# Performance work log

Hardware: AMD Instinct MI355X
Metric: run time of the kernel (lower is better)

The kernel has to match this reference:

```python
import jax, jax.numpy as jnp
import numpy as np

N_F, N_C = 100000, 25000          # fine / coarse node counts
C_IN, C_OUT = 128, 128
E_POOL, E = 200000, 400000        # pooling edges, coarse point-point edges


def setup_inputs() -> dict:
    key = jax.random.key(0)
    ks = jax.random.split(key, 12)
    x = jax.random.normal(ks[0], (N_F, C_IN), jnp.float32)
    # pooling edges: src in fine graph, dst in coarse graph
    pool_src = jax.random.randint(ks[1], (E_POOL,), 0, N_F, dtype=jnp.int64)
    pool_dst = jax.random.randint(ks[2], (E_POOL,), 0, N_C, dtype=jnp.int64)
    pool_edge_index = jnp.stack([pool_src, pool_dst])
    pool_edge_attr = jax.random.uniform(ks[3], (E_POOL,), jnp.float32)
    # coarse point-point edges
    src = jax.random.randint(ks[4], (E,), 0, N_C, dtype=jnp.int64)
    dst = jax.random.randint(ks[5], (E,), 0, N_C, dtype=jnp.int64)
    edge_index = jnp.stack([src, dst])
    edge_attr = jax.random.uniform(ks[6], (E,), jnp.float32)
    s_in = 1.0 / np.sqrt(C_IN).astype(np.float32)
    s_out = 1.0 / np.sqrt(C_OUT).astype(np.float32)
    W1_root = jax.random.normal(ks[7], (C_IN, C_OUT), jnp.float32) * s_in
    W1_nb = jax.random.normal(ks[8], (C_IN, C_OUT), jnp.float32) * s_in
    b1 = jnp.zeros((C_OUT,), jnp.float32)
    W2_root = jax.random.normal(ks[9], (C_OUT, C_OUT), jnp.float32) * s_out
    W2_nb = jax.random.normal(ks[10], (C_OUT, C_OUT), jnp.float32) * s_out
    b2 = jnp.zeros((C_OUT,), jnp.float32)
    return {
        "x": x,
        "pool_edge_index": pool_edge_index,
        "pool_edge_attr": pool_edge_attr,
        "edge_index": edge_index,
        "edge_attr": edge_attr,
        "W1_root": W1_root, "W1_nb": W1_nb, "b1": b1,
        "W2_root": W2_root, "W2_nb": W2_nb, "b2": b2,
        "n_coarse": N_C,
    }


def _graph_conv(h, edge_index, edge_attr, W_root, W_nb, b, n_nodes):
    # GraphConv with edge weights: out = h @ W_root + scatter_add(w_e * (h[src] @ W_nb), dst) + b
    msg = edge_attr[:, None] * (h[edge_index[0]] @ W_nb)          # [E, C_out]
    agg = jax.ops.segment_sum(msg, edge_index[1], num_segments=n_nodes)
    return h @ W_root + agg + b


def reference(x, pool_edge_index, pool_edge_attr, edge_index, edge_attr,
              W1_root, W1_nb, b1, W2_root, W2_nb, b2, n_coarse):
    # CustomPoolingAdd: weighted scatter-add fine -> coarse
    pooled = jax.ops.segment_sum(pool_edge_attr[:, None] * x[pool_edge_index[0]],
                                 pool_edge_index[1], num_segments=n_coarse)  # [N_c, C_in]
    h = _graph_conv(pooled, edge_index, edge_attr, W1_root, W1_nb, b1, n_coarse)
    h = _graph_conv(h, edge_index, edge_attr, W2_root, W2_nb, b2, n_coarse)
    return h
```

## Files before the change

### kernel.cpp

```cpp
#include <hip/hip_runtime.h>

typedef __attribute__((ext_vector_type(8))) short   short8;
typedef __attribute__((ext_vector_type(8))) __bf16  bf16x8;
typedef __attribute__((ext_vector_type(4))) float   f32x4;

__device__ __forceinline__ float bf2f(unsigned short u) {
    union { unsigned int i; float f; } v; v.i = ((unsigned int)u) << 16; return v.f;
}
__device__ __forceinline__ unsigned short f2bf(float f) {
    union { float f; unsigned int i; } v; v.f = f;
    unsigned int r = v.i + 0x7fffu + ((v.i >> 16) & 1u);
    return (unsigned short)(r >> 16);
}

__device__ __forceinline__ int load_idx(const void* p, int is64, long long i) {
    return is64 ? (int)((const long long*)p)[i] : ((const int*)p)[i];
}
__device__ __forceinline__ float load_f(const void* p, int isbf, long long i) {
    return isbf ? bf2f(((const unsigned short*)p)[i]) : ((const float*)p)[i];
}

__device__ __forceinline__ int self_is64(const int* p) {
    int lane = threadIdx.x & 63;
    unsigned long long b = __ballot(p[2 * lane + 1] != 0);
    return b == 0ull;
}
__device__ __forceinline__ int self_isbf(const unsigned int* p) {
    int lane = threadIdx.x & 63;
    unsigned int lo = p[lane] & 0xFFFFu;
    int e = (int)((lo >> 7) & 0xFF);
    int ok = (lo == 0u) || (e >= 88 && e <= 141);
    return (__ballot(!ok) == 0ull) ? 1 : 0;
}

__global__ void detect_kernel(const int* __restrict__ pei, const int* __restrict__ ei,
                              const unsigned int* f0, const unsigned int* f1,
                              const unsigned int* f2, const unsigned int* f3,
                              const unsigned int* f4, const unsigned int* f5,
                              const unsigned int* f6, const unsigned int* f7,
                              const unsigned int* f8,
                              int* __restrict__ flags) {
    int lane = threadIdx.x & 63;
    unsigned long long ba = __ballot(pei[2 * lane + 1] != 0);
    unsigned long long bb = __ballot(ei[2 * lane + 1] != 0);
    const unsigned int* fa[9] = {f0, f1, f2, f3, f4, f5, f6, f7, f8};
    int bf[9];
    #pragma unroll
    for (int t = 0; t < 9; t++) {
        unsigned int lo = fa[t][lane] & 0xFFFFu;
        int e = (int)((lo >> 7) & 0xFF);
        int ok = (lo == 0u) || (e >= 88 && e <= 141);
        bf[t] = (__ballot(!ok) == 0ull) ? 1 : 0;
    }
    if (lane == 0) {
        flags[0] = (ba == 0ull);
        flags[1] = (bb == 0ull);
        #pragma unroll
        for (int t = 0; t < 9; t++) flags[2 + t] = bf[t];
    }
}

#define BKT_CAP 64
#define OVF_CAP 4096

__global__ void fillb_kernel(const void* __restrict__ pei, const void* __restrict__ pattr,
                             const void* __restrict__ ei, const void* __restrict__ eattr,
                             int* __restrict__ pcnt, int2* __restrict__ pbkt,
                             int* __restrict__ povfc, int4* __restrict__ povf,
                             int* __restrict__ ccnt, int2* __restrict__ cbkt,
                             int* __restrict__ covfc, int4* __restrict__ covf,
                             int Ep, int Ec) {
    long long g = (long long)blockIdx.x * 256 + threadIdx.x;
    if (g < Ep) {
        int is64 = self_is64((const int*)pei);
        int abf = self_isbf((const unsigned int*)pattr);
        int s = load_idx(pei, is64, g);
        int d = load_idx(pei, is64, (long long)Ep + g);
        float w = load_f(pattr, abf, g);
        int pos = atomicAdd(&pcnt[d], 1);
        if (pos < BKT_CAP) {
            pbkt[(long long)d * BKT_CAP + pos] = make_int2(s, __float_as_int(w));
        } else {
            int oi = atomicAdd(povfc, 1);
            if (oi < OVF_CAP) povf[oi] = make_int4(s, __float_as_int(w), d, 0);
        }
    } else if (g - Ep < Ec) {
        long long e = g - Ep;
        int is64 = self_is64((const int*)ei);
        int abf = self_isbf((const unsigned int*)eattr);
        int s = load_idx(ei, is64, e);
        int d = load_idx(ei, is64, (long long)Ec + e);
        float w = load_f(eattr, abf, e);
        int pos = atomicAdd(&ccnt[d], 1);
        if (pos < BKT_CAP) {
            cbkt[(long long)d * BKT_CAP + pos] = make_int2(s, __float_as_int(w));
        } else {
            int oi = atomicAdd(covfc, 1);
            if (oi < OVF_CAP) covf[oi] = make_int4(s, __float_as_int(w), d, 0);
        }
    }
}

__global__ void gatherb_kernel(const void* __restrict__ in,
                               const int* __restrict__ cnt,
                               const int2* __restrict__ bkt,
                               const int* __restrict__ ovfc,
                               const int4* __restrict__ ovf,
                               unsigned short* __restrict__ out, int NC,
                               int detectIn) {
    int d = blockIdx.x * 4 + (threadIdx.x >> 6);
    if (d >= NC) return;
    int lane = threadIdx.x & 63;
    int j1 = cnt[d]; if (j1 > BKT_CAP) j1 = BKT_CAP;
    const int2* row = bkt + (long long)d * BKT_CAP;
    float ax = 0.f, ay = 0.f;
    int bf = detectIn ? self_isbf((const unsigned int*)in) : 1;
    if (!bf) {
        const float* fin = (const float*)in;
        int c0 = lane * 2;
        int j = 0;
        for (; j + 4 <= j1; j += 4) {
            int2 e0 = row[j], e1 = row[j + 1], e2 = row[j + 2], e3 = row[j + 3];
            float w0 = __int_as_float(e0.y), w1 = __int_as_float(e1.y);
            float w2 = __int_as_float(e2.y), w3 = __int_as_float(e3.y);
            float2 v0 = *(const float2*)(fin + (long long)e0.x * 128 + c0);
            float2 v1 = *(const float2*)(fin + (long long)e1.x * 128 + c0);
            float2 v2 = *(const float2*)(fin + (long long)e2.x * 128 + c0);
            float2 v3 = *(const float2*)(fin + (long long)e3.x * 128 + c0);
            ax += w0 * v0.x + w1 * v1.x + w2 * v2.x + w3 * v3.x;
            ay += w0 * v0.y + w1 * v1.y + w2 * v2.y + w3 * v3.y;
        }
        for (; j < j1; j++) {
            int2 e = row[j];
            float w = __int_as_float(e.y);
            float2 v = *(const float2*)(fin + (long long)e.x * 128 + c0);
            ax += w * v.x; ay += w * v.y;
        }
        int novf = *ovfc;
        if (novf > 0) {
            if (novf > OVF_CAP) novf = OVF_CAP;
            for (int k = 0; k < novf; k++) {
                int4 e = ovf[k];
                if (e.z == d) {
                    float w = __int_as_float(e.y);
                    float2 v = *(const float2*)(fin + (long long)e.x * 128 + c0);
                    ax += w * v.x; ay += w * v.y;
                }
            }
        }
    } else {
        const unsigned int* uin = (const unsigned int*)in;
        int j = 0;
        for (; j + 4 <= j1; j += 4) {
            int2 e0 = row[j], e1 = row[j + 1], e2 = row[j + 2], e3 = row[j + 3];
            float w0 = __int_as_float(e0.y), w1 = __int_as_float(e1.y);
            float w2 = __int_as_float(e2.y), w3 = __int_as_float(e3.y);
            unsigned int v0 = uin[(long long)e0.x * 64 + lane];
            unsigned int v1 = uin[(long long)e1.x * 64 + lane];
            unsigned int v2 = uin[(long long)e2.x * 64 + lane];
            unsigned int v3 = uin[(long long)e3.x * 64 + lane];
            ax += w0 * bf2f((unsigned short)v0) + w1 * bf2f((unsigned short)v1)
                + w2 * bf2f((unsigned short)v2) + w3 * bf2f((unsigned short)v3);
            ay += w0 * bf2f((unsigned short)(v0 >> 16)) + w1 * bf2f((unsigned short)(v1 >> 16))
                + w2 * bf2f((unsigned short)(v2 >> 16)) + w3 * bf2f((unsigned short)(v3 >> 16));
        }
        for (; j < j1; j++) {
            int2 e = row[j];
            float w = __int_as_float(e.y);
            unsigned int v = uin[(long long)e.x * 64 + lane];
            ax += w * bf2f((unsigned short)v);
            ay += w * bf2f((unsigned short)(v >> 16));
        }
        int novf = *ovfc;
        if (novf > 0) {
            if (novf > OVF_CAP) novf = OVF_CAP;
            for (int k = 0; k < novf; k++) {
                int4 e = ovf[k];
                if (e.z == d) {
                    float w = __int_as_float(e.y);
                    unsigned int v = uin[(long long)e.x * 64 + lane];
                    ax += w * bf2f((unsigned short)v);
                    ay += w * bf2f((unsigned short)(v >> 16));
                }
            }
        }
    }
    unsigned int o = (unsigned int)f2bf(ax) | ((unsigned int)f2bf(ay) << 16);
    ((unsigned int*)out)[(long long)d * 64 + lane] = o;
}

__global__ void packw_kernel(const void* __restrict__ w1r, const void* __restrict__ w1n,
                             const void* __restrict__ w2r, const void* __restrict__ w2n,
                             unsigned short* __restrict__ wpack) {
    int gid = blockIdx.x * 256 + threadIdx.x;
    int layer = gid >> 15;
    int r = gid & 32767;
    int j = r & 7, lane = (r >> 3) & 63, ch = (r >> 9) & 7, ct = (r >> 12) & 7;
    int n = ct * 16 + (lane & 15);
    int k = ch * 32 + (lane >> 4) * 8 + j;
    const void* w;
    if (layer == 0) w = (k < 128) ? w1r : w1n;
    else            w = (k < 128) ? w2r : w2n;
    int fs = self_isbf((const unsigned int*)w);
    float v = load_f(w, fs, (long long)(k & 127) * 128 + n);
    wpack[gid] = f2bf(v);
}

__global__ __launch_bounds__(256, 4)
void gemm_mfma_kernel(const unsigned short* __restrict__ H,
                      const unsigned short* __restrict__ G,
                      const unsigned short* __restrict__ wpack,
                      const void* __restrict__ bias,
                      float* __restrict__ outF, unsigned short* __restrict__ outB,
                      int NC) {
    __shared__ unsigned short ldsA[64 * 264];
    int tid = threadIdx.x;
    long long r0 = (long long)blockIdx.x * 64;
    for (int i = tid; i < 4096; i += 256) {
        int mat = i >> 11;
        int flat = i & 2047;
        int row = flat >> 5;
        int c4 = flat & 31;
        long long r = r0 + row;
        const unsigned short* srcp = mat ? G : H;
        uint2 v = make_uint2(0u, 0u);
        if (r < NC) v = *(const uint2*)(srcp + r * 128 + c4 * 4);
        *(uint2*)&ldsA[row * 264 + mat * 128 + c4 * 4] = v;
    }
    __syncthreads();

    int wave = tid >> 6, lane = tid & 63;
    int m = lane & 15, quad = lane >> 4;
    int arow = wave * 16 + m;

    bf16x8 a[8];
    #pragma unroll
    for (int ch = 0; ch < 8; ch++) {
        short8 av = *(const short8*)&ldsA[arow * 264 + ch * 32 + quad * 8];
        a[ch] = __builtin_bit_cast(bf16x8, av);
    }

    f32x4 acc[8];
    #pragma unroll
    for (int ct = 0; ct < 8; ct++) acc[ct] = (f32x4){0.f, 0.f, 0.f, 0.f};

    #pragma unroll
    for (int ct = 0; ct < 8; ct++) {
        #pragma unroll
        for (int ch = 0; ch < 8; ch++) {
            short8 bv = *(const short8*)(wpack + ((ct * 8 + ch) * 64 + lane) * 8);
            acc[ct] = __builtin_amdgcn_mfma_f32_16x16x32_bf16(
                a[ch], __builtin_bit_cast(bf16x8, bv), acc[ct], 0, 0, 0);
        }
    }

    int bbf = self_isbf((const unsigned int*)bias);
    #pragma unroll
    for (int ct = 0; ct < 8; ct++) {
        int n = ct * 16 + m;
        float bv = load_f(bias, bbf, n);
        #pragma unroll
        for (int r = 0; r < 4; r++) {
            long long rr = r0 + wave * 16 + quad * 4 + r;
            if (rr < NC) {
                float val = acc[ct][r] + bv;
                if (outF) outF[rr * 128 + n] = val;
                else      outB[rr * 128 + n] = f2bf(val);
            }
        }
    }
}

__global__ void pool_scatter_kernel(const void* __restrict__ x, const void* __restrict__ pei,
                                    const void* __restrict__ pattr, const int* __restrict__ flags,
                                    float* __restrict__ pooled, int Ep, int CI) {
    int c = blockIdx.y * blockDim.x + threadIdx.x;
    if (c >= CI) return;
    int e = blockIdx.x;
    int is64 = flags[0], xbf = flags[2], abf = flags[3];
    int s = load_idx(pei, is64, e);
    int d = load_idx(pei, is64, (long long)Ep + e);
    float w = load_f(pattr, abf, e);
    float v = load_f(x, xbf, (long long)s * CI + c);
    atomicAdd(&pooled[(long long)d * CI + c], w * v);
}

__global__ void conv_scatter_kernel(const float* __restrict__ t, const void* __restrict__ ei,
                                    const void* __restrict__ attr, const int* __restrict__ flags,
                                    float* __restrict__ outacc, int Ec, int CO) {
    int c = blockIdx.y * blockDim.x + threadIdx.x;
    if (c >= CO) return;
    int e = blockIdx.x;
    int is64 = flags[1], abf = flags[4];
    int s = load_idx(ei, is64, e);
    int d = load_idx(ei, is64, (long long)Ec + e);
    float w = load_f(attr, abf, e);
    atomicAdd(&outacc[(long long)d * CO + c], w * t[(long long)s * CO + c]);
}

__global__ void gemm_kernel(const float* H, const void* __restrict__ Wr,
                            const void* __restrict__ Wn, const void* __restrict__ bias,
                            const int* __restrict__ flags, int fWr, int fWn, int fB,
                            float* out_root, float* out_t, int NC, int CI, int CO) {
    __shared__ float lds[4][1024];
    int wave = threadIdx.x >> 6;
    int lane = threadIdx.x & 63;
    int r = blockIdx.x * 4 + wave;
    if (r < NC) {
        const float* hrow = H + (long long)r * CI;
        for (int k = lane; k < CI; k += 64) lds[wave][k] = hrow[k];
    }
    __syncthreads();
    if (r >= NC) return;
    int wrbf = flags[fWr], wnbf = flags[fWn], bbf = flags[fB];
    for (int c0 = lane * 2; c0 < CO; c0 += 128) {
        int two = (c0 + 1 < CO);
        float ar0 = 0.f, ar1 = 0.f, an0 = 0.f, an1 = 0.f;
        for (int k = 0; k < CI; k++) {
            float h = lds[wave][k];
            ar0 += h * load_f(Wr, wrbf, (long long)k * CO + c0);
            an0 += h * load_f(Wn, wnbf, (long long)k * CO + c0);
            if (two) {
                ar1 += h * load_f(Wr, wrbf, (long long)k * CO + c0 + 1);
                an1 += h * load_f(Wn, wnbf, (long long)k * CO + c0 + 1);
            }
        }
        long long o = (long long)r * CO + c0;
        out_root[o] = ar0 + load_f(bias, bbf, c0);
        out_t[o] = an0;
        if (two) {
            out_root[o + 1] = ar1 + load_f(bias, bbf, c0 + 1);
            out_t[o + 1] = an1;
        }
    }
}

__global__ void to_out_kernel(const float* __restrict__ in, float* __restrict__ out, long long n) {
    long long stride = (long long)gridDim.x * blockDim.x;
    for (long long i = (long long)blockIdx.x * blockDim.x + threadIdx.x; i < n; i += stride)
        out[i] = in[i];
}

extern "C" void kernel_launch(void* const* d_in, const int* in_sizes, int n_in,
                              void* d_out, int out_size, void* d_ws, size_t ws_size,
                              hipStream_t stream) {
    const void* x = d_in[0]; const void* pei = d_in[1]; const void* pattr = d_in[2];
    const void* ei = d_in[3]; const void* eattr = d_in[4];
    const void* w1r = d_in[5]; const void* w1n = d_in[6]; const void* b1 = d_in[7];
    const void* w2r = d_in[8]; const void* w2n = d_in[9]; const void* b2 = d_in[10];

    long long CO = in_sizes[7];
    long long CI = CO > 0 ? in_sizes[5] / CO : 0;
    long long Ep = in_sizes[2];
    long long Ec = in_sizes[4];
    long long NC = CO > 0 ? (long long)out_size / CO : 0;
    int sane = (CO > 0 && CI > 0 && CI <= 1024 && CO <= 1024 &&
                CI * CO == in_sizes[5] && NC * CO == out_size &&
                Ep > 0 && Ec > 0 && in_sizes[0] % CI == 0);
    if (!sane) { CO = 128; CI = 128; Ep = 200000; Ec = 400000; NC = 25000; }

    char* ws = (char*)d_ws;

    if (CI == 128 && CO == 128) {
        size_t off = 0;
        unsigned short* bufP = (unsigned short*)(ws + off); off += (size_t)NC * 128 * 2;
        unsigned short* bufH = (unsigned short*)(ws + off); off += (size_t)NC * 128 * 2;
        unsigned short* bufG = (unsigned short*)(ws + off); off += (size_t)NC * 128 * 2;
        unsigned short* wpack = (unsigned short*)(ws + off); off += 65536 * 2;
        int* pcnt  = (int*)(ws + off); off += NC * 4;
        int* ccnt  = (int*)(ws + off); off += NC * 4;
        int* povfc = (int*)(ws + off); off += 4;
        int* covfc = (int*)(ws + off); off += 4;
        off = (off + 15) & ~(size_t)15;
        int4* povf = (int4*)(ws + off); off += (size_t)OVF_CAP * 16;
        int4* covf = (int4*)(ws + off); off += (size_t)OVF_CAP * 16;
        int2* pbkt = (int2*)(ws + off); off += (size_t)NC * BKT_CAP * 8;
        int2* cbkt = (int2*)(ws + off); off += (size_t)NC * BKT_CAP * 8;

        hipMemsetAsync(pcnt, 0, (2 * NC + 2) * 4, stream);

        packw_kernel<<<256, 256, 0, stream>>>(w1r, w1n, w2r, w2n, wpack);

        int gE = (int)((Ep + Ec + 255) / 256);
        fillb_kernel<<<gE, 256, 0, stream>>>(pei, pattr, ei, eattr,
                                             pcnt, pbkt, povfc, povf,
                                             ccnt, cbkt, covfc, covf, (int)Ep, (int)Ec);

        int gN4 = (int)((NC + 3) / 4);
        int gN64 = (int)((NC + 63) / 64);
        gatherb_kernel<<<gN4, 256, 0, stream>>>(x, pcnt, pbkt, povfc, povf, bufP, (int)NC, 1);
        gatherb_kernel<<<gN4, 256, 0, stream>>>(bufP, ccnt, cbkt, covfc, covf, bufG, (int)NC, 0);
        gemm_mfma_kernel<<<gN64, 256, 0, stream>>>(bufP, bufG, wpack, b1,
                                                   nullptr, bufH, (int)NC);
        gatherb_kernel<<<gN4, 256, 0, stream>>>(bufH, ccnt, cbkt, covfc, covf, bufG, (int)NC, 0);
        gemm_mfma_kernel<<<gN64, 256, 0, stream>>>(bufH, bufG, wpack + 32768, b2,
                                                   (float*)d_out, nullptr, (int)NC);
        return;
    }

    size_t szP = (size_t)NC * CI * sizeof(float);
    size_t szO = (size_t)NC * CO * sizeof(float);
    float *bufP, *bufA, *bufB, *bufC; int* flags;
    if (CI == CO) {
        bufP = (float*)ws; bufA = (float*)(ws + szP);
        bufB = bufP; bufC = bufA;
        flags = (int*)(ws + szP + szO);
    } else {
        bufP = (float*)ws; bufA = (float*)(ws + szP);
        bufB = (float*)(ws + szP + szO); bufC = (float*)(ws + szP + 2 * szO);
        flags = (int*)(ws + szP + 3 * szO);
    }
    detect_kernel<<<1, 64, 0, stream>>>(
        (const int*)pei, (const int*)ei,
        (const unsigned int*)x, (const unsigned int*)pattr, (const unsigned int*)eattr,
        (const unsigned int*)w1r, (const unsigned int*)w1n, (const unsigned int*)b1,
        (const unsigned int*)w2r, (const unsigned int*)w2n, (const unsigned int*)b2,
        flags);
    hipMemsetAsync(bufP, 0, szP, stream);
    int blkP = (CI % 64 == 0 && CI <= 256) ? (int)CI : 256;
    int blkC = (CO % 64 == 0 && CO <= 256) ? (int)CO : 256;
    dim3 gP((unsigned)Ep, (unsigned)((CI + blkP - 1) / blkP));
    dim3 gC((unsigned)Ec, (unsigned)((CO + blkC - 1) / blkC));
    int gG = (int)((NC + 3) / 4);
    pool_scatter_kernel<<<gP, blkP, 0, stream>>>(x, pei, pattr, flags, bufP, (int)Ep, (int)CI);
    if (CI == CO) {
        gemm_kernel<<<gG, 256, 0, stream>>>(bufP, w1r, w1n, b1, flags, 5, 6, 7,
                                            bufA, bufP, (int)NC, (int)CI, (int)CO);
        conv_scatter_kernel<<<gC, blkC, 0, stream>>>(bufP, ei, eattr, flags, bufA, (int)Ec, (int)CO);
        gemm_kernel<<<gG, 256, 0, stream>>>(bufA, w2r, w2n, b2, flags, 8, 9, 10,
                                            bufP, bufA, (int)NC, (int)CO, (int)CO);
        conv_scatter_kernel<<<gC, blkC, 0, stream>>>(bufA, ei, eattr, flags, bufP, (int)Ec, (int)CO);
        to_out_kernel<<<4096, 256, 0, stream>>>(bufP, (float*)d_out, NC * CO);
    } else {
        gemm_kernel<<<gG, 256, 0, stream>>>(bufP, w1r, w1n, b1, flags, 5, 6, 7,
                                            bufA, bufB, (int)NC, (int)CI, (int)CO);
        conv_scatter_kernel<<<gC, blkC, 0, stream>>>(bufB, ei, eattr, flags, bufA, (int)Ec, (int)CO);
        gemm_kernel<<<gG, 256, 0, stream>>>(bufA, w2r, w2n, b2, flags, 8, 9, 10,
                                            bufB, bufC, (int)NC, (int)CO, (int)CO);
        conv_scatter_kernel<<<gC, blkC, 0, stream>>>(bufC, ei, eattr, flags, bufB, (int)Ec, (int)CO);
        to_out_kernel<<<4096, 256, 0, stream>>>(bufB, (float*)d_out, NC * CO);
    }
}
```

Before: 239.7 us.

## Fuse weight packing into bucket fill, pad counters, unroll gathers by eight

The weight-packing kernel is merged into the edge bucket-fill kernel as extra trailing blocks, which removes one kernel launch. Per-node atomic counters are padded to a stride of 16 ints so counters for neighbouring nodes sit on separate 64-byte lines, meant to reduce atomic contention. The gather loops are unrolled to eight edges per step so more independent row loads are in flight. In exchange, the counter arrays and the memset grow sixteenfold, and the larger unroll raises register pressure.

```diff
diff --git a/kernel.cpp b/kernel.cpp
--- a/kernel.cpp
+++ b/kernel.cpp
@@ -62,14 +62,33 @@
 
 #define BKT_CAP 64
 #define OVF_CAP 4096
-
-__global__ void fillb_kernel(const void* __restrict__ pei, const void* __restrict__ pattr,
-                             const void* __restrict__ ei, const void* __restrict__ eattr,
-                             int* __restrict__ pcnt, int2* __restrict__ pbkt,
-                             int* __restrict__ povfc, int4* __restrict__ povf,
-                             int* __restrict__ ccnt, int2* __restrict__ cbkt,
-                             int* __restrict__ covfc, int4* __restrict__ covf,
-                             int Ep, int Ec) {
+#define CNT_STRIDE 16
+
+__global__ void fillpack_kernel(const void* __restrict__ pei, const void* __restrict__ pattr,
+                                const void* __restrict__ ei, const void* __restrict__ eattr,
+                                int* __restrict__ pcnt, int2* __restrict__ pbkt,
+                                int* __restrict__ povfc, int4* __restrict__ povf,
+                                int* __restrict__ ccnt, int2* __restrict__ cbkt,
+                                int* __restrict__ covfc, int4* __restrict__ covf,
+                                int Ep, int Ec, int gE,
+                                const void* __restrict__ w1r, const void* __restrict__ w1n,
+                                const void* __restrict__ w2r, const void* __restrict__ w2n,
+                                unsigned short* __restrict__ wpack) {
+    if ((int)blockIdx.x >= gE) {
+        int gid = ((int)blockIdx.x - gE) * 256 + threadIdx.x;
+        int layer = gid >> 15;
+        int r = gid & 32767;
+        int j = r & 7, lane = (r >> 3) & 63, ch = (r >> 9) & 7, ct = (r >> 12) & 7;
+        int n = ct * 16 + (lane & 15);
+        int k = ch * 32 + (lane >> 4) * 8 + j;
+        const void* w;
+        if (layer == 0) w = (k < 128) ? w1r : w1n;
+        else            w = (k < 128) ? w2r : w2n;
+        int fs = self_isbf((const unsigned int*)w);
+        float v = load_f(w, fs, (long long)(k & 127) * 128 + n);
+        wpack[gid] = f2bf(v);
+        return;
+    }
     long long g = (long long)blockIdx.x * 256 + threadIdx.x;
     if (g < Ep) {
         int is64 = self_is64((const int*)pei);
@@ -77,7 +96,7 @@
         int s = load_idx(pei, is64, g);
         int d = load_idx(pei, is64, (long long)Ep + g);
         float w = load_f(pattr, abf, g);
-        int pos = atomicAdd(&pcnt[d], 1);
+        int pos = atomicAdd(&pcnt[d * CNT_STRIDE], 1);
         if (pos < BKT_CAP) {
             pbkt[(long long)d * BKT_CAP + pos] = make_int2(s, __float_as_int(w));
         } else {
@@ -91,7 +110,7 @@
         int s = load_idx(ei, is64, e);
         int d = load_idx(ei, is64, (long long)Ec + e);
         float w = load_f(eattr, abf, e);
-        int pos = atomicAdd(&ccnt[d], 1);
+        int pos = atomicAdd(&ccnt[d * CNT_STRIDE], 1);
         if (pos < BKT_CAP) {
             cbkt[(long long)d * BKT_CAP + pos] = make_int2(s, __float_as_int(w));
         } else {
@@ -111,7 +130,7 @@
     int d = blockIdx.x * 4 + (threadIdx.x >> 6);
     if (d >= NC) return;
     int lane = threadIdx.x & 63;
-    int j1 = cnt[d]; if (j1 > BKT_CAP) j1 = BKT_CAP;
+    int j1 = cnt[d * CNT_STRIDE]; if (j1 > BKT_CAP) j1 = BKT_CAP;
     const int2* row = bkt + (long long)d * BKT_CAP;
     float ax = 0.f, ay = 0.f;
     int bf = detectIn ? self_isbf((const unsigned int*)in) : 1;
@@ -119,16 +138,36 @@
         const float* fin = (const float*)in;
         int c0 = lane * 2;
         int j = 0;
-        for (; j + 4 <= j1; j += 4) {
+        for (; j + 8 <= j1; j += 8) {
             int2 e0 = row[j], e1 = row[j + 1], e2 = row[j + 2], e3 = row[j + 3];
-            float w0 = __int_as_float(e0.y), w1 = __int_as_float(e1.y);
-            float w2 = __int_as_float(e2.y), w3 = __int_as_float(e3.y);
+            int2 e4 = row[j + 4], e5 = row[j + 5], e6 = row[j + 6], e7 = row[j + 7];
             float2 v0 = *(const float2*)(fin + (long long)e0.x * 128 + c0);
             float2 v1 = *(const float2*)(fin + (long long)e1.x * 128 + c0);
             float2 v2 = *(const float2*)(fin + (long long)e2.x * 128 + c0);
             float2 v3 = *(const float2*)(fin + (long long)e3.x * 128 + c0);
-            ax += w0 * v0.x + w1 * v1.x + w2 * v2.x + w3 * v3.x;
-            ay += w0 * v0.y + w1 * v1.y + w2 * v2.y + w3 * v3.y;
+            float2 v4 = *(const float2*)(fin + (long long)e4.x * 128 + c0);
+            float2 v5 = *(const float2*)(fin + (long long)e5.x * 128 + c0);
+            float2 v6 = *(const float2*)(fin + (long long)e6.x * 128 + c0);
+            float2 v7 = *(const float2*)(fin + (long long)e7.x * 128 + c0);
+            ax += __int_as_float(e0.y) * v0.x + __int_as_float(e1.y) * v1.x
+                + __int_as_float(e2.y) * v2.x + __int_as_float(e3.y) * v3.x
+                + __int_as_float(e4.y) * v4.x + __int_as_float(e5.y) * v5.x
+                + __int_as_float(e6.y) * v6.x + __int_as_float(e7.y) * v7.x;
+            ay += __int_as_float(e0.y) * v0.y + __int_as_float(e1.y) * v1.y
+                + __int_as_float(e2.y) * v2.y + __int_as_float(e3.y) * v3.y
+                + __int_as_float(e4.y) * v4.y + __int_as_float(e5.y) * v5.y
+                + __int_as_float(e6.y) * v6.y + __int_as_float(e7.y) * v7.y;
+        }
+        for (; j + 4 <= j1; j += 4) {
+            int2 e0 = row[j], e1 = row[j + 1], e2 = row[j + 2], e3 = row[j + 3];
+            float2 v0 = *(const float2*)(fin + (long long)e0.x * 128 + c0);
+            float2 v1 = *(const float2*)(fin + (long long)e1.x * 128 + c0);
+            float2 v2 = *(const float2*)(fin + (long long)e2.x * 128 + c0);
+            float2 v3 = *(const float2*)(fin + (long long)e3.x * 128 + c0);
+            ax += __int_as_float(e0.y) * v0.x + __int_as_float(e1.y) * v1.x
+                + __int_as_float(e2.y) * v2.x + __int_as_float(e3.y) * v3.x;
+            ay += __int_as_float(e0.y) * v0.y + __int_as_float(e1.y) * v1.y
+                + __int_as_float(e2.y) * v2.y + __int_as_float(e3.y) * v3.y;
         }
         for (; j < j1; j++) {
             int2 e = row[j];
@@ -151,18 +190,48 @@
     } else {
         const unsigned int* uin = (const unsigned int*)in;
         int j = 0;
-        for (; j + 4 <= j1; j += 4) {
+        for (; j + 8 <= j1; j += 8) {
             int2 e0 = row[j], e1 = row[j + 1], e2 = row[j + 2], e3 = row[j + 3];
-            float w0 = __int_as_float(e0.y), w1 = __int_as_float(e1.y);
-            float w2 = __int_as_float(e2.y), w3 = __int_as_float(e3.y);
+            int2 e4 = row[j + 4], e5 = row[j + 5], e6 = row[j + 6], e7 = row[j + 7];
             unsigned int v0 = uin[(long long)e0.x * 64 + lane];
             unsigned int v1 = uin[(long long)e1.x * 64 + lane];
             unsigned int v2 = uin[(long long)e2.x * 64 + lane];
             unsigned int v3 = uin[(long long)e3.x * 64 + lane];
-            ax += w0 * bf2f((unsigned short)v0) + w1 * bf2f((unsigned short)v1)
-                + w2 * bf2f((unsigned short)v2) + w3 * bf2f((unsigned short)v3);
-            ay += w0 * bf2f((unsigned short)(v0 >> 16)) + w1 * bf2f((unsigned short)(v1 >> 16))
-                + w2 * bf2f((unsigned short)(v2 >> 16)) + w3 * bf2f((unsigned short)(v3 >> 16));
+            unsigned int v4 = uin[(long long)e4.x * 64 + lane];
+            unsigned int v5 = uin[(long long)e5.x * 64 + lane];
+            unsigned int v6 = uin[(long long)e6.x * 64 + lane];
+            unsigned int v7 = uin[(long long)e7.x * 64 + lane];
+            ax += __int_as_float(e0.y) * bf2f((unsigned short)v0)
+                + __int_as_float(e1.y) * bf2f((unsigned short)v1)
+                + __int_as_float(e2.y) * bf2f((unsigned short)v2)
+                + __int_as_float(e3.y) * bf2f((unsigned short)v3)
+                + __int_as_float(e4.y) * bf2f((unsigned short)v4)
+                + __int_as_float(e5.y) * bf2f((unsigned short)v5)
+                + __int_as_float(e6.y) * bf2f((unsigned short)v6)
+                + __int_as_float(e7.y) * bf2f((unsigned short)v7);
+            ay += __int_as_float(e0.y) * bf2f((unsigned short)(v0 >> 16))
+                + __int_as_float(e1.y) * bf2f((unsigned short)(v1 >> 16))
+                + __int_as_float(e2.y) * bf2f((unsigned short)(v2 >> 16))
+                + __int_as_float(e3.y) * bf2f((unsigned short)(v3 >> 16))
+                + __int_as_float(e4.y) * bf2f((unsigned short)(v4 >> 16))
+                + __int_as_float(e5.y) * bf2f((unsigned short)(v5 >> 16))
+                + __int_as_float(e6.y) * bf2f((unsigned short)(v6 >> 16))
+                + __int_as_float(e7.y) * bf2f((unsigned short)(v7 >> 16));
+        }
+        for (; j + 4 <= j1; j += 4) {
+            int2 e0 = row[j], e1 = row[j + 1], e2 = row[j + 2], e3 = row[j + 3];
+            unsigned int v0 = uin[(long long)e0.x * 64 + lane];
+            unsigned int v1 = uin[(long long)e1.x * 64 + lane];
+            unsigned int v2 = uin[(long long)e2.x * 64 + lane];
+            unsigned int v3 = uin[(long long)e3.x * 64 + lane];
+            ax += __int_as_float(e0.y) * bf2f((unsigned short)v0)
+                + __int_as_float(e1.y) * bf2f((unsigned short)v1)
+                + __int_as_float(e2.y) * bf2f((unsigned short)v2)
+                + __int_as_float(e3.y) * bf2f((unsigned short)v3);
+            ay += __int_as_float(e0.y) * bf2f((unsigned short)(v0 >> 16))
+                + __int_as_float(e1.y) * bf2f((unsigned short)(v1 >> 16))
+                + __int_as_float(e2.y) * bf2f((unsigned short)(v2 >> 16))
+                + __int_as_float(e3.y) * bf2f((unsigned short)(v3 >> 16));
         }
         for (; j < j1; j++) {
             int2 e = row[j];
@@ -187,23 +256,6 @@
     }
     unsigned int o = (unsigned int)f2bf(ax) | ((unsigned int)f2bf(ay) << 16);
     ((unsigned int*)out)[(long long)d * 64 + lane] = o;
-}
-
-__global__ void packw_kernel(const void* __restrict__ w1r, const void* __restrict__ w1n,
-                             const void* __restrict__ w2r, const void* __restrict__ w2n,
-                             unsigned short* __restrict__ wpack) {
-    int gid = blockIdx.x * 256 + threadIdx.x;
-    int layer = gid >> 15;
-    int r = gid & 32767;
-    int j = r & 7, lane = (r >> 3) & 63, ch = (r >> 9) & 7, ct = (r >> 12) & 7;
-    int n = ct * 16 + (lane & 15);
-    int k = ch * 32 + (lane >> 4) * 8 + j;
-    const void* w;
-    if (layer == 0) w = (k < 128) ? w1r : w1n;
-    else            w = (k < 128) ? w2r : w2n;
-    int fs = self_isbf((const unsigned int*)w);
-    float v = load_f(w, fs, (long long)(k & 127) * 128 + n);
-    wpack[gid] = f2bf(v);
 }
 
 __global__ __launch_bounds__(256, 4)
@@ -367,8 +419,8 @@
         unsigned short* bufH = (unsigned short*)(ws + off); off += (size_t)NC * 128 * 2;
         unsigned short* bufG = (unsigned short*)(ws + off); off += (size_t)NC * 128 * 2;
         unsigned short* wpack = (unsigned short*)(ws + off); off += 65536 * 2;
-        int* pcnt  = (int*)(ws + off); off += NC * 4;
-        int* ccnt  = (int*)(ws + off); off += NC * 4;
+        int* pcnt  = (int*)(ws + off); off += NC * CNT_STRIDE * 4;
+        int* ccnt  = (int*)(ws + off); off += NC * CNT_STRIDE * 4;
         int* povfc = (int*)(ws + off); off += 4;
         int* covfc = (int*)(ws + off); off += 4;
         off = (off + 15) & ~(size_t)15;
@@ -377,14 +429,14 @@
         int2* pbkt = (int2*)(ws + off); off += (size_t)NC * BKT_CAP * 8;
         int2* cbkt = (int2*)(ws + off); off += (size_t)NC * BKT_CAP * 8;
 
-        hipMemsetAsync(pcnt, 0, (2 * NC + 2) * 4, stream);
-
-        packw_kernel<<<256, 256, 0, stream>>>(w1r, w1n, w2r, w2n, wpack);
+        hipMemsetAsync(pcnt, 0, (2 * NC * CNT_STRIDE + 2) * 4, stream);
 
         int gE = (int)((Ep + Ec + 255) / 256);
-        fillb_kernel<<<gE, 256, 0, stream>>>(pei, pattr, ei, eattr,
-                                             pcnt, pbkt, povfc, povf,
-                                             ccnt, cbkt, covfc, covf, (int)Ep, (int)Ec);
+        fillpack_kernel<<<gE + 256, 256, 0, stream>>>(pei, pattr, ei, eattr,
+                                                      pcnt, pbkt, povfc, povf,
+                                                      ccnt, cbkt, covfc, covf,
+                                                      (int)Ep, (int)Ec, gE,
+                                                      w1r, w1n, w2r, w2n, wpack);
 
         int gN4 = (int)((NC + 3) / 4);
         int gN64 = (int)((NC + 63) / 64);
```

Result: no change. 235.0 us (-2.0%).

## Split wave into half-waves for wider gathers, merge weight packing into fill

Applied to the files above, without the earlier changes.

Each gather wave now splits into two 32-lane halves that process alternating edges with 8- or 16-byte vector loads per lane, then combine their partial sums with a cross-half shuffle. The intermediate gathers use 8 edges in flight per half, and the pooling bucket capacity shrinks to 32 to cut bucket memory. Weight packing is folded into the fill kernel as extra blocks, which removes one launch. The goal is more memory-level parallelism on random row gathers and less launch overhead. The cost is more registers, and the smaller pooling buckets push more high-degree nodes onto the slow overflow path.

```diff
diff --git a/kernel.cpp b/kernel.cpp
--- a/kernel.cpp
+++ b/kernel.cpp
@@ -60,17 +60,37 @@
     }
 }
 
-#define BKT_CAP 64
+#define PBKT_CAP 32
+#define CBKT_CAP 64
 #define OVF_CAP 4096
 
-__global__ void fillb_kernel(const void* __restrict__ pei, const void* __restrict__ pattr,
-                             const void* __restrict__ ei, const void* __restrict__ eattr,
-                             int* __restrict__ pcnt, int2* __restrict__ pbkt,
-                             int* __restrict__ povfc, int4* __restrict__ povf,
-                             int* __restrict__ ccnt, int2* __restrict__ cbkt,
-                             int* __restrict__ covfc, int4* __restrict__ covf,
-                             int Ep, int Ec) {
-    long long g = (long long)blockIdx.x * 256 + threadIdx.x;
+__global__ void fillpack_kernel(const void* __restrict__ pei, const void* __restrict__ pattr,
+                                const void* __restrict__ ei, const void* __restrict__ eattr,
+                                int* __restrict__ pcnt, int2* __restrict__ pbkt,
+                                int* __restrict__ povfc, int4* __restrict__ povf,
+                                int* __restrict__ ccnt, int2* __restrict__ cbkt,
+                                int* __restrict__ covfc, int4* __restrict__ covf,
+                                int Ep, int Ec, int gE,
+                                const void* __restrict__ w1r, const void* __restrict__ w1n,
+                                const void* __restrict__ w2r, const void* __restrict__ w2n,
+                                unsigned short* __restrict__ wpack) {
+    int bid = (int)blockIdx.x;
+    if (bid >= gE) {
+        int gid = (bid - gE) * 256 + threadIdx.x;
+        int layer = gid >> 15;
+        int r = gid & 32767;
+        int j = r & 7, lane = (r >> 3) & 63, ch = (r >> 9) & 7, ct = (r >> 12) & 7;
+        int n = ct * 16 + (lane & 15);
+        int k = ch * 32 + (lane >> 4) * 8 + j;
+        const void* w;
+        if (layer == 0) w = (k < 128) ? w1r : w1n;
+        else            w = (k < 128) ? w2r : w2n;
+        int fs = self_isbf((const unsigned int*)w);
+        float v = load_f(w, fs, (long long)(k & 127) * 128 + n);
+        wpack[gid] = f2bf(v);
+        return;
+    }
+    long long g = (long long)bid * 256 + threadIdx.x;
     if (g < Ep) {
         int is64 = self_is64((const int*)pei);
         int abf = self_isbf((const unsigned int*)pattr);
@@ -78,8 +98,8 @@
         int d = load_idx(pei, is64, (long long)Ep + g);
         float w = load_f(pattr, abf, g);
         int pos = atomicAdd(&pcnt[d], 1);
-        if (pos < BKT_CAP) {
-            pbkt[(long long)d * BKT_CAP + pos] = make_int2(s, __float_as_int(w));
+        if (pos < PBKT_CAP) {
+            pbkt[(long long)d * PBKT_CAP + pos] = make_int2(s, __float_as_int(w));
         } else {
             int oi = atomicAdd(povfc, 1);
             if (oi < OVF_CAP) povf[oi] = make_int4(s, __float_as_int(w), d, 0);
@@ -92,8 +112,8 @@
         int d = load_idx(ei, is64, (long long)Ec + e);
         float w = load_f(eattr, abf, e);
         int pos = atomicAdd(&ccnt[d], 1);
-        if (pos < BKT_CAP) {
-            cbkt[(long long)d * BKT_CAP + pos] = make_int2(s, __float_as_int(w));
+        if (pos < CBKT_CAP) {
+            cbkt[(long long)d * CBKT_CAP + pos] = make_int2(s, __float_as_int(w));
         } else {
             int oi = atomicAdd(covfc, 1);
             if (oi < OVF_CAP) covf[oi] = make_int4(s, __float_as_int(w), d, 0);
@@ -101,41 +121,171 @@
     }
 }
 
-__global__ void gatherb_kernel(const void* __restrict__ in,
+
+__global__ void gatherx_kernel(const void* __restrict__ x,
                                const int* __restrict__ cnt,
                                const int2* __restrict__ bkt,
                                const int* __restrict__ ovfc,
                                const int4* __restrict__ ovf,
-                               unsigned short* __restrict__ out, int NC,
-                               int detectIn) {
+                               unsigned short* __restrict__ out, int NC) {
     int d = blockIdx.x * 4 + (threadIdx.x >> 6);
     if (d >= NC) return;
     int lane = threadIdx.x & 63;
-    int j1 = cnt[d]; if (j1 > BKT_CAP) j1 = BKT_CAP;
-    const int2* row = bkt + (long long)d * BKT_CAP;
-    float ax = 0.f, ay = 0.f;
-    int bf = detectIn ? self_isbf((const unsigned int*)in) : 1;
-    if (!bf) {
-        const float* fin = (const float*)in;
-        int c0 = lane * 2;
-        int j = 0;
-        for (; j + 4 <= j1; j += 4) {
-            int2 e0 = row[j], e1 = row[j + 1], e2 = row[j + 2], e3 = row[j + 3];
+    int half = lane >> 5, l = lane & 31;
+    int j1 = cnt[d]; if (j1 > PBKT_CAP) j1 = PBKT_CAP;
+    const int2* row = bkt + (long long)d * PBKT_CAP;
+    float a0 = 0.f, a1 = 0.f, a2 = 0.f, a3 = 0.f;
+    int xisbf = self_isbf((const unsigned int*)x);
+    if (xisbf) {
+        const uint2* uin = (const uint2*)x;
+        int j = half;
+        for (; j + 6 < j1; j += 8) {
+            int2 e0 = row[j], e1 = row[j + 2], e2 = row[j + 4], e3 = row[j + 6];
+            uint2 v0 = uin[(long long)e0.x * 32 + l];
+            uint2 v1 = uin[(long long)e1.x * 32 + l];
+            uint2 v2 = uin[(long long)e2.x * 32 + l];
+            uint2 v3 = uin[(long long)e3.x * 32 + l];
             float w0 = __int_as_float(e0.y), w1 = __int_as_float(e1.y);
             float w2 = __int_as_float(e2.y), w3 = __int_as_float(e3.y);
-            float2 v0 = *(const float2*)(fin + (long long)e0.x * 128 + c0);
-            float2 v1 = *(const float2*)(fin + (long long)e1.x * 128 + c0);
-            float2 v2 = *(const float2*)(fin + (long long)e2.x * 128 + c0);
-            float2 v3 = *(const float2*)(fin + (long long)e3.x * 128 + c0);
-            ax += w0 * v0.x + w1 * v1.x + w2 * v2.x + w3 * v3.x;
-            ay += w0 * v0.y + w1 * v1.y + w2 * v2.y + w3 * v3.y;
-        }
-        for (; j < j1; j++) {
+            a0 += w0 * bf2f((unsigned short)v0.x) + w1 * bf2f((unsigned short)v1.x)
+                + w2 * bf2f((unsigned short)v2.x) + w3 * bf2f((unsigned short)v3.x);
+            a1 += w0 * bf2f((unsigned short)(v0.x >> 16)) + w1 * bf2f((unsigned short)(v1.x >> 16))
+                + w2 * bf2f((unsigned short)(v2.x >> 16)) + w3 * bf2f((unsigned short)(v3.x >> 16));
+            a2 += w0 * bf2f((unsigned short)v0.y) + w1 * bf2f((unsigned short)v1.y)
+                + w2 * bf2f((unsigned short)v2.y) + w3 * bf2f((unsigned short)v3.y);
+            a3 += w0 * bf2f((unsigned short)(v0.y >> 16)) + w1 * bf2f((unsigned short)(v1.y >> 16))
+                + w2 * bf2f((unsigned short)(v2.y >> 16)) + w3 * bf2f((unsigned short)(v3.y >> 16));
+        }
+        for (; j < j1; j += 2) {
             int2 e = row[j];
             float w = __int_as_float(e.y);
-            float2 v = *(const float2*)(fin + (long long)e.x * 128 + c0);
-            ax += w * v.x; ay += w * v.y;
-        }
+            uint2 v = uin[(long long)e.x * 32 + l];
+            a0 += w * bf2f((unsigned short)v.x);
+            a1 += w * bf2f((unsigned short)(v.x >> 16));
+            a2 += w * bf2f((unsigned short)v.y);
+            a3 += w * bf2f((unsigned short)(v.y >> 16));
+        }
+        if (half == 0) {
+            int novf = *ovfc;
+            if (novf > 0) {
+                if (novf > OVF_CAP) novf = OVF_CAP;
+                for (int k = 0; k < novf; k++) {
+                    int4 e = ovf[k];
+                    if (e.z == d) {
+                        float w = __int_as_float(e.y);
+                        uint2 v = uin[(long long)e.x * 32 + l];
+                        a0 += w * bf2f((unsigned short)v.x);
+                        a1 += w * bf2f((unsigned short)(v.x >> 16));
+                        a2 += w * bf2f((unsigned short)v.y);
+                        a3 += w * bf2f((unsigned short)(v.y >> 16));
+                    }
+                }
+            }
+        }
+    } else {
+        const float4* fin = (const float4*)x;
+        int j = half;
+        for (; j + 6 < j1; j += 8) {
+            int2 e0 = row[j], e1 = row[j + 2], e2 = row[j + 4], e3 = row[j + 6];
+            float4 v0 = fin[(long long)e0.x * 32 + l];
+            float4 v1 = fin[(long long)e1.x * 32 + l];
+            float4 v2 = fin[(long long)e2.x * 32 + l];
+            float4 v3 = fin[(long long)e3.x * 32 + l];
+            float w0 = __int_as_float(e0.y), w1 = __int_as_float(e1.y);
+            float w2 = __int_as_float(e2.y), w3 = __int_as_float(e3.y);
+            a0 += w0 * v0.x + w1 * v1.x + w2 * v2.x + w3 * v3.x;
+            a1 += w0 * v0.y + w1 * v1.y + w2 * v2.y + w3 * v3.y;
+            a2 += w0 * v0.z + w1 * v1.z + w2 * v2.z + w3 * v3.z;
+            a3 += w0 * v0.w + w1 * v1.w + w2 * v2.w + w3 * v3.w;
+        }
+        for (; j < j1; j += 2) {
+            int2 e = row[j];
+            float w = __int_as_float(e.y);
+            float4 v = fin[(long long)e.x * 32 + l];
+            a0 += w * v.x; a1 += w * v.y; a2 += w * v.z; a3 += w * v.w;
+        }
+        if (half == 0) {
+            int novf = *ovfc;
+            if (novf > 0) {
+                if (novf > OVF_CAP) novf = OVF_CAP;
+                for (int k = 0; k < novf; k++) {
+                    int4 e = ovf[k];
+                    if (e.z == d) {
+                        float w = __int_as_float(e.y);
+                        float4 v = fin[(long long)e.x * 32 + l];
+                        a0 += w * v.x; a1 += w * v.y; a2 += w * v.z; a3 += w * v.w;
+                    }
+                }
+            }
+        }
+    }
+    a0 += __shfl_xor(a0, 32); a1 += __shfl_xor(a1, 32);
+    a2 += __shfl_xor(a2, 32); a3 += __shfl_xor(a3, 32);
+    if (half == 0) {
+        uint2 o;
+        o.x = (unsigned int)f2bf(a0) | ((unsigned int)f2bf(a1) << 16);
+        o.y = (unsigned int)f2bf(a2) | ((unsigned int)f2bf(a3) << 16);
+        ((uint2*)out)[(long long)d * 32 + l] = o;
+    }
+}
+
+__global__ void gatherb_kernel(const unsigned short* __restrict__ in,
+                               const int* __restrict__ cnt,
+                               const int2* __restrict__ bkt, int cap,
+                               const int* __restrict__ ovfc,
+                               const int4* __restrict__ ovf,
+                               unsigned short* __restrict__ out, int NC) {
+    int d = blockIdx.x * 4 + (threadIdx.x >> 6);
+    if (d >= NC) return;
+    int lane = threadIdx.x & 63;
+    int half = lane >> 5, l = lane & 31;
+    int j1 = cnt[d]; if (j1 > cap) j1 = cap;
+    const int2* row = bkt + (long long)d * cap;
+    const uint2* uin = (const uint2*)in;
+    float a0 = 0.f, a1 = 0.f, a2 = 0.f, a3 = 0.f;
+    int j = half;
+    for (; j + 14 < j1; j += 16) {
+        int2 e0 = row[j],      e1 = row[j + 2],  e2 = row[j + 4],  e3 = row[j + 6];
+        int2 e4 = row[j + 8],  e5 = row[j + 10], e6 = row[j + 12], e7 = row[j + 14];
+        uint2 v0 = uin[(long long)e0.x * 32 + l];
+        uint2 v1 = uin[(long long)e1.x * 32 + l];
+        uint2 v2 = uin[(long long)e2.x * 32 + l];
+        uint2 v3 = uin[(long long)e3.x * 32 + l];
+        uint2 v4 = uin[(long long)e4.x * 32 + l];
+        uint2 v5 = uin[(long long)e5.x * 32 + l];
+        uint2 v6 = uin[(long long)e6.x * 32 + l];
+        uint2 v7 = uin[(long long)e7.x * 32 + l];
+        float w0 = __int_as_float(e0.y), w1 = __int_as_float(e1.y);
+        float w2 = __int_as_float(e2.y), w3 = __int_as_float(e3.y);
+        float w4 = __int_as_float(e4.y), w5 = __int_as_float(e5.y);
+        float w6 = __int_as_float(e6.y), w7 = __int_as_float(e7.y);
+        a0 += w0 * bf2f((unsigned short)v0.x) + w1 * bf2f((unsigned short)v1.x)
+            + w2 * bf2f((unsigned short)v2.x) + w3 * bf2f((unsigned short)v3.x)
+            + w4 * bf2f((unsigned short)v4.x) + w5 * bf2f((unsigned short)v5.x)
+            + w6 * bf2f((unsigned short)v6.x) + w7 * bf2f((unsigned short)v7.x);
+        a1 += w0 * bf2f((unsigned short)(v0.x >> 16)) + w1 * bf2f((unsigned short)(v1.x >> 16))
+            + w2 * bf2f((unsigned short)(v2.x >> 16)) + w3 * bf2f((unsigned short)(v3.x >> 16))
+            + w4 * bf2f((unsigned short)(v4.x >> 16)) + w5 * bf2f((unsigned short)(v5.x >> 16))
+            + w6 * bf2f((unsigned short)(v6.x >> 16)) + w7 * bf2f((unsigned short)(v7.x >> 16));
+        a2 += w0 * bf2f((unsigned short)v0.y) + w1 * bf2f((unsigned short)v1.y)
+            + w2 * bf2f((unsigned short)v2.y) + w3 * bf2f((unsigned short)v3.y)
+            + w4 * bf2f((unsigned short)v4.y) + w5 * bf2f((unsigned short)v5.y)
+            + w6 * bf2f((unsigned short)v6.y) + w7 * bf2f((unsigned short)v7.y);
+        a3 += w0 * bf2f((unsigned short)(v0.y >> 16)) + w1 * bf2f((unsigned short)(v1.y >> 16))
+            + w2 * bf2f((unsigned short)(v2.y >> 16)) + w3 * bf2f((unsigned short)(v3.y >> 16))
+            + w4 * bf2f((unsigned short)(v4.y >> 16)) + w5 * bf2f((unsigned short)(v5.y >> 16))
+            + w6 * bf2f((unsigned short)(v6.y >> 16)) + w7 * bf2f((unsigned short)(v7.y >> 16));
+    }
+    for (; j < j1; j += 2) {
+        int2 e = row[j];
+        float w = __int_as_float(e.y);
+        uint2 v = uin[(long long)e.x * 32 + l];
+        a0 += w * bf2f((unsigned short)v.x);
+        a1 += w * bf2f((unsigned short)(v.x >> 16));
+        a2 += w * bf2f((unsigned short)v.y);
+        a3 += w * bf2f((unsigned short)(v.y >> 16));
+    }
+    if (half == 0) {
         int novf = *ovfc;
         if (novf > 0) {
             if (novf > OVF_CAP) novf = OVF_CAP;
@@ -143,67 +293,23 @@
                 int4 e = ovf[k];
                 if (e.z == d) {
                     float w = __int_as_float(e.y);
-                    float2 v = *(const float2*)(fin + (long long)e.x * 128 + c0);
-                    ax += w * v.x; ay += w * v.y;
+                    uint2 v = uin[(long long)e.x * 32 + l];
+                    a0 += w * bf2f((unsigned short)v.x);
+                    a1 += w * bf2f((unsigned short)(v.x >> 16));
+                    a2 += w * bf2f((unsigned short)v.y);
+                    a3 += w * bf2f((unsigned short)(v.y >> 16));
                 }
             }
         }
-    } else {
-        const unsigned int* uin = (const unsigned int*)in;
-        int j = 0;
-        for (; j + 4 <= j1; j += 4) {
-            int2 e0 = row[j], e1 = row[j + 1], e2 = row[j + 2], e3 = row[j + 3];
-            float w0 = __int_as_float(e0.y), w1 = __int_as_float(e1.y);
-            float w2 = __int_as_float(e2.y), w3 = __int_as_float(e3.y);
-            unsigned int v0 = uin[(long long)e0.x * 64 + lane];
-            unsigned int v1 = uin[(long long)e1.x * 64 + lane];
-            unsigned int v2 = uin[(long long)e2.x * 64 + lane];
-            unsigned int v3 = uin[(long long)e3.x * 64 + lane];
-            ax += w0 * bf2f((unsigned short)v0) + w1 * bf2f((unsigned short)v1)
-                + w2 * bf2f((unsigned short)v2) + w3 * bf2f((unsigned short)v3);
-            ay += w0 * bf2f((unsigned short)(v0 >> 16)) + w1 * bf2f((unsigned short)(v1 >> 16))
-                + w2 * bf2f((unsigned short)(v2 >> 16)) + w3 * bf2f((unsigned short)(v3 >> 16));
-        }
-        for (; j < j1; j++) {
-            int2 e = row[j];
-            float w = __int_as_float(e.y);
-            unsigned int v = uin[(long long)e.x * 64 + lane];
-            ax += w * bf2f((unsigned short)v);
-            ay += w * bf2f((unsigned short)(v >> 16));
-        }
-        int novf = *ovfc;
-        if (novf > 0) {
-            if (novf > OVF_CAP) novf = OVF_CAP;
-            for (int k = 0; k < novf; k++) {
-                int4 e = ovf[k];
-                if (e.z == d) {
-                    float w = __int_as_float(e.y);
-                    unsigned int v = uin[(long long)e.x * 64 + lane];
-                    ax += w * bf2f((unsigned short)v);
-                    ay += w * bf2f((unsigned short)(v >> 16));
-                }
-            }
-        }
-    }
-    unsigned int o = (unsigned int)f2bf(ax) | ((unsigned int)f2bf(ay) << 16);
-    ((unsigned int*)out)[(long long)d * 64 + lane] = o;
-}
-
-__global__ void packw_kernel(const void* __restrict__ w1r, const void* __restrict__ w1n,
-                             const void* __restrict__ w2r, const void* __restrict__ w2n,
-                             unsigned short* __restrict__ wpack) {
-    int gid = blockIdx.x * 256 + threadIdx.x;
-    int layer = gid >> 15;
-    int r = gid & 32767;
-    int j = r & 7, lane = (r >> 3) & 63, ch = (r >> 9) & 7, ct = (r >> 12) & 7;
-    int n = ct * 16 + (lane & 15);
-    int k = ch * 32 + (lane >> 4) * 8 + j;
-    const void* w;
-    if (layer == 0) w = (k < 128) ? w1r : w1n;
-    else            w = (k < 128) ? w2r : w2n;
-    int fs = self_isbf((const unsigned int*)w);
-    float v = load_f(w, fs, (long long)(k & 127) * 128 + n);
-    wpack[gid] = f2bf(v);
+    }
+    a0 += __shfl_xor(a0, 32); a1 += __shfl_xor(a1, 32);
+    a2 += __shfl_xor(a2, 32); a3 += __shfl_xor(a3, 32);
+    if (half == 0) {
+        uint2 o;
+        o.x = (unsigned int)f2bf(a0) | ((unsigned int)f2bf(a1) << 16);
+        o.y = (unsigned int)f2bf(a2) | ((unsigned int)f2bf(a3) << 16);
+        ((uint2*)out)[(long long)d * 32 + l] = o;
+    }
 }
 
 __global__ __launch_bounds__(256, 4)
@@ -374,25 +480,28 @@
         off = (off + 15) & ~(size_t)15;
         int4* povf = (int4*)(ws + off); off += (size_t)OVF_CAP * 16;
         int4* covf = (int4*)(ws + off); off += (size_t)OVF_CAP * 16;
-        int2* pbkt = (int2*)(ws + off); off += (size_t)NC * BKT_CAP * 8;
-        int2* cbkt = (int2*)(ws + off); off += (size_t)NC * BKT_CAP * 8;
+        int2* pbkt = (int2*)(ws + off); off += (size_t)NC * PBKT_CAP * 8;
+        int2* cbkt = (int2*)(ws + off); off += (size_t)NC * CBKT_CAP * 8;
 
         hipMemsetAsync(pcnt, 0, (2 * NC + 2) * 4, stream);
 
-        packw_kernel<<<256, 256, 0, stream>>>(w1r, w1n, w2r, w2n, wpack);
-
         int gE = (int)((Ep + Ec + 255) / 256);
-        fillb_kernel<<<gE, 256, 0, stream>>>(pei, pattr, ei, eattr,
-                                             pcnt, pbkt, povfc, povf,
-                                             ccnt, cbkt, covfc, covf, (int)Ep, (int)Ec);
+        fillpack_kernel<<<gE + 256, 256, 0, stream>>>(
+            pei, pattr, ei, eattr,
+            pcnt, pbkt, povfc, povf,
+            ccnt, cbkt, covfc, covf,
+            (int)Ep, (int)Ec, gE,
+            w1r, w1n, w2r, w2n, wpack);
 
         int gN4 = (int)((NC + 3) / 4);
         int gN64 = (int)((NC + 63) / 64);
-        gatherb_kernel<<<gN4, 256, 0, stream>>>(x, pcnt, pbkt, povfc, povf, bufP, (int)NC, 1);
-        gatherb_kernel<<<gN4, 256, 0, stream>>>(bufP, ccnt, cbkt, covfc, covf, bufG, (int)NC, 0);
+        gatherx_kernel<<<gN4, 256, 0, stream>>>(x, pcnt, pbkt, povfc, povf, bufP, (int)NC);
+        gatherb_kernel<<<gN4, 256, 0, stream>>>(bufP, ccnt, cbkt, CBKT_CAP, covfc, covf,
+                                                bufG, (int)NC);
         gemm_mfma_kernel<<<gN64, 256, 0, stream>>>(bufP, bufG, wpack, b1,
                                                    nullptr, bufH, (int)NC);
-        gatherb_kernel<<<gN4, 256, 0, stream>>>(bufH, ccnt, cbkt, covfc, covf, bufG, (int)NC, 0);
+        gatherb_kernel<<<gN4, 256, 0, stream>>>(bufH, ccnt, cbkt, CBKT_CAP, covfc, covf,
+                                                bufG, (int)NC);
         gemm_mfma_kernel<<<gN64, 256, 0, stream>>>(bufH, bufG, wpack + 32768, b2,
                                                    (float*)d_out, nullptr, (int)NC);
         return;
```

Result: no change. 239.8 us (+0.1%).
